# Kernel tuning notes

Measured on AMD Instinct MI355X. Metric: run time of the kernel, lower is better.

The kernel has to match this reference:

```python
import jax, jax.numpy as jnp
import numpy as np

B, T, H = 2048, 784, 64
STATE_DIM = 1
IN_DIM = 1 + STATE_DIM  # concat([t, y])
INNER_LR = 0.01
NUM_GRAD_STEPS = 4


def _unif(k, shape, fan_in):
    lim = 1.0 / np.sqrt(fan_in)
    return jax.random.uniform(k, shape, jnp.float32, -lim, lim)


def setup_inputs() -> dict:
    key = jax.random.key(0)
    ks = jax.random.split(key, 8)
    ts = (jnp.arange(T, dtype=jnp.float32) / T)
    xs = jax.random.normal(ks[0], (B, T), jnp.float32)
    mask = jax.random.bernoulli(ks[1], 0.5, (B, T - 1))  # teacher-forcing draws
    # equinox Linear default init: U(-1/sqrt(fan_in), 1/sqrt(fan_in)) for W and b
    W1 = _unif(ks[2], (H, IN_DIM), IN_DIM)
    b1 = _unif(ks[3], (H,), IN_DIM)
    W2 = _unif(ks[4], (H, H), H)
    b2 = _unif(ks[5], (H,), H)
    W3 = _unif(ks[6], (STATE_DIM, H), H)
    b3 = _unif(ks[7], (STATE_DIM,), H)
    return {"ts": ts, "xs": xs, "mask": mask,
            "W1": W1, "b1": b1, "W2": W2, "b2": b2, "W3": W3, "b3": b3}


def _mlp(theta, t, y):
    # theta: tuple of (W1,b1,W2,b2,W3,b3); t, y scalars -> output (state_dim,)
    W1, b1, W2, b2, W3, b3 = theta
    h = jnp.stack([t, y])                # (2,)
    h = jnp.tanh(W1 @ h + b1)            # (H,)
    h = jnp.tanh(W2 @ h + b2)            # (H,)
    return W3 @ h + b3                   # (state_dim,)


def reference(ts, xs, mask, W1, b1, W2, b2, W3, b3):
    theta0 = (W1, b1, W2, b2, W3, b3)

    def forward(xs_row, mask_row):
        def step(carry, inp):
            theta, t_prev, x_hat, x_prev = carry
            x_true, t_curr, m = inp
            x_t = jnp.where(m, x_true, x_hat)  # bernoulli(0.5) teacher forcing

            def inner_loss(th):
                pred = _mlp(th, t_curr, x_prev)
                return jnp.mean((pred - x_t) ** 2)

            for _ in range(NUM_GRAD_STEPS):
                g = jax.grad(inner_loss)(theta)
                theta = jax.tree_util.tree_map(
                    lambda p, gr: p - INNER_LR * gr, theta, g)

            deltat = t_curr - t_prev
            x_hat_new = _mlp(theta, t_curr + deltat, x_true).squeeze()
            return (theta, t_curr, x_hat_new, x_true), x_hat_new

        init = (theta0, ts[0], xs_row[0], xs_row[0])
        _, x_hats = jax.lax.scan(step, init, (xs_row[1:], ts[1:], mask_row))
        return jnp.concatenate([xs_row[:1], x_hats], axis=0)  # (T,)

    return jax.vmap(forward)(xs, mask)  # (B, T)
```

## Files before the change

kernel.cpp:

```cpp
#include <hip/hip_runtime.h>
#include <math.h>


#define TT  784
#define HH  64
#define LR  0.01f

typedef _Float16 h2v __attribute__((ext_vector_type(2)));
#define FDOT2(a, b, c) __builtin_amdgcn_fdot2((a), (b), (c), false)
#define BC(f) __builtin_bit_cast(h2v, (f))

__device__ __forceinline__ float fast_tanh(float x) {
    float e = __builtin_amdgcn_exp2f(x * 2.885390081777926814f);
    float r = __builtin_amdgcn_rcpf(e + 1.0f);
    return fmaf(-2.0f, r, 1.0f);
}

template <int CTRL, int RMASK, bool BC_>
__device__ __forceinline__ float dpp_add(float x) {
    int t = __builtin_amdgcn_update_dpp(0, __builtin_bit_cast(int, x),
                                        CTRL, RMASK, 0xf, BC_);
    return x + __builtin_bit_cast(float, t);
}

__device__ __forceinline__ float wave_sum(float x) {
    x = dpp_add<0x111, 0xf, true>(x);
    x = dpp_add<0x112, 0xf, true>(x);
    x = dpp_add<0x114, 0xf, true>(x);
    x = dpp_add<0x118, 0xf, true>(x);
    x = dpp_add<0x142, 0xa, false>(x);
    x = dpp_add<0x143, 0xc, false>(x);
    return __builtin_bit_cast(float,
        __builtin_amdgcn_readlane(__builtin_bit_cast(int, x), 63));
}

__global__ __launch_bounds__(64, 2)
void ttt_kernel(const float* __restrict__ ts,
                const float* __restrict__ xs,
                const int*   __restrict__ mask,
                const float* __restrict__ W1,
                const float* __restrict__ b1,
                const float* __restrict__ W2,
                const float* __restrict__ b2,
                const float* __restrict__ W3,
                const float* __restrict__ b3,
                float* __restrict__ out)
{
    __shared__ __align__(16) _Float16 s_h1h[HH];
    __shared__ __align__(16) _Float16 s_dzh[HH];
    __shared__ float s_ts[TT];
    __shared__ float s_xs[TT];
    __shared__ int   s_mask[TT - 1];

    const int row  = blockIdx.x;
    const int lane = threadIdx.x;

    for (int i = lane; i < TT; i += HH) {
        s_ts[i] = ts[i];
        s_xs[i] = xs[row * TT + i];
    }
    for (int i = lane; i < TT - 1; i += HH) s_mask[i] = mask[row * (TT - 1) + i];

    float w1a = W1[2 * lane + 0];
    float w1b = W1[2 * lane + 1];
    float b1v = b1[lane];
    float b2v = b2[lane];
    float w3v = W3[lane];
    float b3v = b3[0];

    h2v w2r[HH / 2];
    h2v w2c[HH / 2];
#pragma unroll
    for (int k = 0; k < HH / 2; ++k) {
        w2r[k] = h2v{(_Float16)W2[lane * HH + 2 * k], (_Float16)W2[lane * HH + 2 * k + 1]};
        w2c[k] = h2v{(_Float16)W2[(2 * k) * HH + lane], (_Float16)W2[(2 * k + 1) * HH + lane]};
    }
    __syncthreads();

    const float4* h1v4 = (const float4*)s_h1h;
    const float4* dzv4 = (const float4*)s_dzh;

    float t_prev = s_ts[0];
    const float x0 = s_xs[0];
    float x_hat  = x0;
    float x_prev = x0;
    if (lane == 0) out[row * TT] = x0;

    float4 hr[8];
    float  h1f, h2f, predf;
    float  z1f;
    float  sdz1 = 0.f;
    float  tc = 0.f, x_true = 0.f, tin = 0.f, nls = 0.f;

    auto FWD_TAIL = [&]() {
        float a0 = 0.f, a1 = 0.f, a2 = 0.f, a3 = 0.f;
#pragma unroll
        for (int k = 0; k < 8; ++k) {
            float4 q = h1v4[k];
            hr[k] = q;
            a0 = FDOT2(w2r[4 * k + 0], BC(q.x), a0);
            a1 = FDOT2(w2r[4 * k + 1], BC(q.y), a1);
            a2 = FDOT2(w2r[4 * k + 2], BC(q.z), a2);
            a3 = FDOT2(w2r[4 * k + 3], BC(q.w), a3);
        }
        float z2 = ((a0 + a1) + (a2 + a3)) + b2v;
        h2f = fast_tanh(z2);
        predf = wave_sum(w3v * h2f) + b3v;
    };

    auto MERGED = [&](float xt, bool final_) {
        const float dl   = 2.0f * (predf - xt);
        const float dz2s = dl * w3v * (1.0f - h2f * h2f);
        s_dzh[lane] = (_Float16)dz2s;
        w3v = fmaf(-LR * dl, h2f, w3v);
        b3v -= LR * dl;
        b2v -= LR * dz2s;
        const _Float16 sd = (_Float16)(-LR * dz2s);
        const h2v sdv = h2v{sd, sd};
        const _Float16 sh = (_Float16)(-LR * h1f);
        const h2v shv = h2v{sh, sh};
#pragma unroll
        for (int k = 0; k < 8; ++k) {
            float4 o = hr[k];
            w2r[4 * k + 0] += sdv * BC(o.x);
            w2r[4 * k + 1] += sdv * BC(o.y);
            w2r[4 * k + 2] += sdv * BC(o.z);
            w2r[4 * k + 3] += sdv * BC(o.w);
        }
        float d0 = 0.f, d1 = 0.f, d2 = 0.f, d3 = 0.f;
#pragma unroll
        for (int k = 0; k < 8; ++k) {
            float4 q = dzv4[k];
            d0 = FDOT2(w2c[4 * k + 0], BC(q.x), d0);
            d1 = FDOT2(w2c[4 * k + 1], BC(q.y), d1);
            d2 = FDOT2(w2c[4 * k + 2], BC(q.z), d2);
            d3 = FDOT2(w2c[4 * k + 3], BC(q.w), d3);
        }
        const float dh1 = (d0 + d1) + (d2 + d3);
        const float dz1 = dh1 * (1.0f - h1f * h1f);
        sdz1 += dz1;
        if (!final_) {
            z1f = fmaf(nls, dz1, z1f);
        } else {
            w1a = fmaf(-LR * tc,     sdz1, w1a);
            w1b = fmaf(-LR * x_prev, sdz1, w1b);
            b1v = fmaf(-LR,          sdz1, b1v);
            z1f = fmaf(w1a, tin, fmaf(w1b, x_true, b1v));
        }
        h1f = fast_tanh(z1f);
        s_h1h[lane] = (_Float16)h1f;
#pragma unroll
        for (int k = 0; k < 8; ++k) {
            float4 q = dzv4[k];
            w2c[4 * k + 0] += shv * BC(q.x);
            w2c[4 * k + 1] += shv * BC(q.y);
            w2c[4 * k + 2] += shv * BC(q.z);
            w2c[4 * k + 3] += shv * BC(q.w);
        }
        float a0 = 0.f, a1 = 0.f, a2 = 0.f, a3 = 0.f;
#pragma unroll
        for (int k = 0; k < 8; ++k) {
            float4 q = h1v4[k];
            hr[k] = q;
            a0 = FDOT2(w2r[4 * k + 0], BC(q.x), a0);
            a1 = FDOT2(w2r[4 * k + 1], BC(q.y), a1);
            a2 = FDOT2(w2r[4 * k + 2], BC(q.z), a2);
            a3 = FDOT2(w2r[4 * k + 3], BC(q.w), a3);
        }
        float z2 = ((a0 + a1) + (a2 + a3)) + b2v;
        h2f = fast_tanh(z2);
        predf = wave_sum(w3v * h2f) + b3v;
    };

    z1f = fmaf(w1a, s_ts[1], fmaf(w1b, x0, b1v));
    h1f = fast_tanh(z1f);
    s_h1h[lane] = (_Float16)h1f;
    FWD_TAIL();

    for (int t = 1; t < TT; ++t) {
        tc     = s_ts[t];
        x_true = s_xs[t];
        tin    = tc + (tc - t_prev);
        nls    = -LR * fmaf(tc, tc, fmaf(x_prev, x_prev, 1.0f));
        const float x_t = s_mask[t - 1] ? x_true : x_hat;

        sdz1 = 0.f;
        MERGED(x_t, false);
        MERGED(x_t, false);
        MERGED(x_t, false);
        MERGED(x_t, true);
        x_hat = predf;

        if (lane == 0) out[row * TT + t] = x_hat;
        t_prev = tc;
        x_prev = x_true;
    }
}

extern "C" void kernel_launch(void* const* d_in, const int* in_sizes, int n_in,
                              void* d_out, int out_size, void* d_ws, size_t ws_size,
                              hipStream_t stream) {
    const float* ts   = (const float*)d_in[0];
    const float* xs   = (const float*)d_in[1];
    const int*   mask = (const int*)d_in[2];
    const float* W1   = (const float*)d_in[3];
    const float* b1   = (const float*)d_in[4];
    const float* W2   = (const float*)d_in[5];
    const float* b2   = (const float*)d_in[6];
    const float* W3   = (const float*)d_in[7];
    const float* b3   = (const float*)d_in[8];
    float* out = (float*)d_out;

    const int B = in_sizes[1] / TT;
    dim3 grid(B), block(HH);
    hipLaunchKernelGGL(ttt_kernel, grid, block, 0, stream,
                       ts, xs, mask, W1, b1, W2, b2, W3, b3, out);
}
```

Measured before the change: 2.523 ms.

## Factor loss scalar out of backward vector, fuse W2 updates, buffer outputs in LDS

```diff
diff --git a/kernel.cpp b/kernel.cpp
--- a/kernel.cpp
+++ b/kernel.cpp
@@ -9,6 +9,7 @@
 typedef _Float16 h2v __attribute__((ext_vector_type(2)));
 #define FDOT2(a, b, c) __builtin_amdgcn_fdot2((a), (b), (c), false)
 #define BC(f) __builtin_bit_cast(h2v, (f))
+#define PKFMA(acc, a, b) acc = __builtin_elementwise_fma((a), (b), (acc))
 
 __device__ __forceinline__ float fast_tanh(float x) {
     float e = __builtin_amdgcn_exp2f(x * 2.885390081777926814f);
@@ -47,9 +48,10 @@
                 float* __restrict__ out)
 {
     __shared__ __align__(16) _Float16 s_h1h[HH];
-    __shared__ __align__(16) _Float16 s_dzh[HH];
+    __shared__ __align__(16) _Float16 s_uh[HH];
     __shared__ float s_ts[TT];
     __shared__ float s_xs[TT];
+    __shared__ float s_out[TT];
     __shared__ int   s_mask[TT - 1];
 
     const int row  = blockIdx.x;
@@ -78,66 +80,48 @@
     __syncthreads();
 
     const float4* h1v4 = (const float4*)s_h1h;
-    const float4* dzv4 = (const float4*)s_dzh;
+    const float4* uv4  = (const float4*)s_uh;
 
     float t_prev = s_ts[0];
     const float x0 = s_xs[0];
     float x_hat  = x0;
     float x_prev = x0;
-    if (lane == 0) out[row * TT] = x0;
+    if (lane == 0) s_out[0] = x0;
 
     float4 hr[8];
     float  h1f, h2f, predf;
+    float  ul;
     float  z1f;
     float  sdz1 = 0.f;
     float  tc = 0.f, x_true = 0.f, tin = 0.f, nls = 0.f;
 
-    auto FWD_TAIL = [&]() {
-        float a0 = 0.f, a1 = 0.f, a2 = 0.f, a3 = 0.f;
-#pragma unroll
-        for (int k = 0; k < 8; ++k) {
-            float4 q = h1v4[k];
-            hr[k] = q;
-            a0 = FDOT2(w2r[4 * k + 0], BC(q.x), a0);
-            a1 = FDOT2(w2r[4 * k + 1], BC(q.y), a1);
-            a2 = FDOT2(w2r[4 * k + 2], BC(q.z), a2);
-            a3 = FDOT2(w2r[4 * k + 3], BC(q.w), a3);
-        }
-        float z2 = ((a0 + a1) + (a2 + a3)) + b2v;
-        h2f = fast_tanh(z2);
-        predf = wave_sum(w3v * h2f) + b3v;
-    };
-
     auto MERGED = [&](float xt, bool final_) {
-        const float dl   = 2.0f * (predf - xt);
-        const float dz2s = dl * w3v * (1.0f - h2f * h2f);
-        s_dzh[lane] = (_Float16)dz2s;
-        w3v = fmaf(-LR * dl, h2f, w3v);
-        b3v -= LR * dl;
-        b2v -= LR * dz2s;
-        const _Float16 sd = (_Float16)(-LR * dz2s);
+        const float diff = predf - xt;
+        const float dl   = diff + diff;
+        const float ndl  = -LR * dl;
+        w3v = fmaf(ndl, h2f, w3v);
+        b3v += ndl;
+        b2v = fmaf(ndl, ul, b2v);
+        const _Float16 sd = (_Float16)(ndl * ul);
         const h2v sdv = h2v{sd, sd};
-        const _Float16 sh = (_Float16)(-LR * h1f);
+        const _Float16 sh = (_Float16)(ndl * h1f);
         const h2v shv = h2v{sh, sh};
-#pragma unroll
-        for (int k = 0; k < 8; ++k) {
-            float4 o = hr[k];
-            w2r[4 * k + 0] += sdv * BC(o.x);
-            w2r[4 * k + 1] += sdv * BC(o.y);
-            w2r[4 * k + 2] += sdv * BC(o.z);
-            w2r[4 * k + 3] += sdv * BC(o.w);
-        }
         float d0 = 0.f, d1 = 0.f, d2 = 0.f, d3 = 0.f;
 #pragma unroll
         for (int k = 0; k < 8; ++k) {
-            float4 q = dzv4[k];
+            float4 q = uv4[k];
             d0 = FDOT2(w2c[4 * k + 0], BC(q.x), d0);
             d1 = FDOT2(w2c[4 * k + 1], BC(q.y), d1);
             d2 = FDOT2(w2c[4 * k + 2], BC(q.z), d2);
             d3 = FDOT2(w2c[4 * k + 3], BC(q.w), d3);
-        }
-        const float dh1 = (d0 + d1) + (d2 + d3);
-        const float dz1 = dh1 * (1.0f - h1f * h1f);
+            PKFMA(w2c[4 * k + 0], shv, BC(q.x));
+            PKFMA(w2c[4 * k + 1], shv, BC(q.y));
+            PKFMA(w2c[4 * k + 2], shv, BC(q.z));
+            PKFMA(w2c[4 * k + 3], shv, BC(q.w));
+        }
+        const float raw = (d0 + d1) + (d2 + d3);
+        const float dh1 = dl * raw;
+        const float dz1 = dh1 * fmaf(-h1f, h1f, 1.0f);
         sdz1 += dz1;
         if (!final_) {
             z1f = fmaf(nls, dz1, z1f);
@@ -151,13 +135,13 @@
         s_h1h[lane] = (_Float16)h1f;
 #pragma unroll
         for (int k = 0; k < 8; ++k) {
-            float4 q = dzv4[k];
-            w2c[4 * k + 0] += shv * BC(q.x);
-            w2c[4 * k + 1] += shv * BC(q.y);
-            w2c[4 * k + 2] += shv * BC(q.z);
-            w2c[4 * k + 3] += shv * BC(q.w);
-        }
-        float a0 = 0.f, a1 = 0.f, a2 = 0.f, a3 = 0.f;
+            float4 o = hr[k];
+            PKFMA(w2r[4 * k + 0], sdv, BC(o.x));
+            PKFMA(w2r[4 * k + 1], sdv, BC(o.y));
+            PKFMA(w2r[4 * k + 2], sdv, BC(o.z));
+            PKFMA(w2r[4 * k + 3], sdv, BC(o.w));
+        }
+        float a0 = b2v, a1 = 0.f, a2 = 0.f, a3 = 0.f;
 #pragma unroll
         for (int k = 0; k < 8; ++k) {
             float4 q = h1v4[k];
@@ -167,15 +151,35 @@
             a2 = FDOT2(w2r[4 * k + 2], BC(q.z), a2);
             a3 = FDOT2(w2r[4 * k + 3], BC(q.w), a3);
         }
-        float z2 = ((a0 + a1) + (a2 + a3)) + b2v;
+        const float z2 = (a0 + a1) + (a2 + a3);
         h2f = fast_tanh(z2);
+        const float uf = w3v * fmaf(-h2f, h2f, 1.0f);
+        ul = uf;
+        s_uh[lane] = (_Float16)uf;
         predf = wave_sum(w3v * h2f) + b3v;
     };
 
     z1f = fmaf(w1a, s_ts[1], fmaf(w1b, x0, b1v));
     h1f = fast_tanh(z1f);
     s_h1h[lane] = (_Float16)h1f;
-    FWD_TAIL();
+    {
+        float a0 = b2v, a1 = 0.f, a2 = 0.f, a3 = 0.f;
+#pragma unroll
+        for (int k = 0; k < 8; ++k) {
+            float4 q = h1v4[k];
+            hr[k] = q;
+            a0 = FDOT2(w2r[4 * k + 0], BC(q.x), a0);
+            a1 = FDOT2(w2r[4 * k + 1], BC(q.y), a1);
+            a2 = FDOT2(w2r[4 * k + 2], BC(q.z), a2);
+            a3 = FDOT2(w2r[4 * k + 3], BC(q.w), a3);
+        }
+        const float z2 = (a0 + a1) + (a2 + a3);
+        h2f = fast_tanh(z2);
+        const float uf = w3v * fmaf(-h2f, h2f, 1.0f);
+        ul = uf;
+        s_uh[lane] = (_Float16)uf;
+        predf = wave_sum(w3v * h2f) + b3v;
+    }
 
     for (int t = 1; t < TT; ++t) {
         tc     = s_ts[t];
@@ -191,10 +195,12 @@
         MERGED(x_t, true);
         x_hat = predf;
 
-        if (lane == 0) out[row * TT + t] = x_hat;
+        if (lane == 0) s_out[t] = x_hat;
         t_prev = tc;
         x_prev = x_true;
     }
+
+    for (int i = lane; i < TT; i += HH) out[row * TT + i] = s_out[i];
 }
 
 extern "C" void kernel_launch(void* const* d_in, const int* in_sizes, int n_in,
```

Result: no change. 2.518 ms (-0.2%).

## Process two batch rows per wavefront with interleaved dependent chains

Applied to the files above, without the earlier changes.

```diff
diff --git a/kernel.cpp b/kernel.cpp
--- a/kernel.cpp
+++ b/kernel.cpp
@@ -9,6 +9,7 @@
 typedef _Float16 h2v __attribute__((ext_vector_type(2)));
 #define FDOT2(a, b, c) __builtin_amdgcn_fdot2((a), (b), (c), false)
 #define BC(f) __builtin_bit_cast(h2v, (f))
+#define PKFMA(acc, a, b) acc = __builtin_elementwise_fma((a), (b), (acc))
 
 __device__ __forceinline__ float fast_tanh(float x) {
     float e = __builtin_amdgcn_exp2f(x * 2.885390081777926814f);
@@ -34,7 +35,7 @@
         __builtin_amdgcn_readlane(__builtin_bit_cast(int, x), 63));
 }
 
-__global__ __launch_bounds__(64, 2)
+__global__ __launch_bounds__(64, 1)
 void ttt_kernel(const float* __restrict__ ts,
                 const float* __restrict__ xs,
                 const int*   __restrict__ mask,
@@ -46,154 +47,234 @@
                 const float* __restrict__ b3,
                 float* __restrict__ out)
 {
-    __shared__ __align__(16) _Float16 s_h1h[HH];
-    __shared__ __align__(16) _Float16 s_dzh[HH];
+    __shared__ __align__(16) _Float16 s_h1h[2][HH];
+    __shared__ __align__(16) _Float16 s_uh[2][HH];
     __shared__ float s_ts[TT];
-    __shared__ float s_xs[TT];
-    __shared__ int   s_mask[TT - 1];
-
-    const int row  = blockIdx.x;
+    __shared__ float s_xs[2][TT];
+    __shared__ float s_out[2][TT];
+    __shared__ int   s_mask[2][TT - 1];
+
+    const int rowA = 2 * blockIdx.x;
+    const int rowB = rowA + 1;
     const int lane = threadIdx.x;
 
     for (int i = lane; i < TT; i += HH) {
-        s_ts[i] = ts[i];
-        s_xs[i] = xs[row * TT + i];
-    }
-    for (int i = lane; i < TT - 1; i += HH) s_mask[i] = mask[row * (TT - 1) + i];
-
-    float w1a = W1[2 * lane + 0];
-    float w1b = W1[2 * lane + 1];
-    float b1v = b1[lane];
-    float b2v = b2[lane];
-    float w3v = W3[lane];
-    float b3v = b3[0];
-
-    h2v w2r[HH / 2];
-    h2v w2c[HH / 2];
+        s_ts[i]    = ts[i];
+        s_xs[0][i] = xs[rowA * TT + i];
+        s_xs[1][i] = xs[rowB * TT + i];
+    }
+    for (int i = lane; i < TT - 1; i += HH) {
+        s_mask[0][i] = mask[rowA * (TT - 1) + i];
+        s_mask[1][i] = mask[rowB * (TT - 1) + i];
+    }
+
+    float w1aA = W1[2 * lane + 0], w1aB = w1aA;
+    float w1bA = W1[2 * lane + 1], w1bB = w1bA;
+    float b1vA = b1[lane], b1vB = b1vA;
+    float b2vA = b2[lane], b2vB = b2vA;
+    float w3vA = W3[lane], w3vB = w3vA;
+    float b3vA = b3[0],    b3vB = b3vA;
+
+    h2v w2rA[HH / 2], w2rB[HH / 2];
+    h2v w2cA[HH / 2], w2cB[HH / 2];
 #pragma unroll
     for (int k = 0; k < HH / 2; ++k) {
-        w2r[k] = h2v{(_Float16)W2[lane * HH + 2 * k], (_Float16)W2[lane * HH + 2 * k + 1]};
-        w2c[k] = h2v{(_Float16)W2[(2 * k) * HH + lane], (_Float16)W2[(2 * k + 1) * HH + lane]};
+        h2v r = h2v{(_Float16)W2[lane * HH + 2 * k], (_Float16)W2[lane * HH + 2 * k + 1]};
+        h2v c = h2v{(_Float16)W2[(2 * k) * HH + lane], (_Float16)W2[(2 * k + 1) * HH + lane]};
+        w2rA[k] = r; w2rB[k] = r;
+        w2cA[k] = c; w2cB[k] = c;
     }
     __syncthreads();
 
-    const float4* h1v4 = (const float4*)s_h1h;
-    const float4* dzv4 = (const float4*)s_dzh;
+    const float4* h1v4A = (const float4*)s_h1h[0];
+    const float4* h1v4B = (const float4*)s_h1h[1];
+    const float4* uv4A  = (const float4*)s_uh[0];
+    const float4* uv4B  = (const float4*)s_uh[1];
 
     float t_prev = s_ts[0];
-    const float x0 = s_xs[0];
-    float x_hat  = x0;
-    float x_prev = x0;
-    if (lane == 0) out[row * TT] = x0;
-
-    float4 hr[8];
-    float  h1f, h2f, predf;
-    float  z1f;
-    float  sdz1 = 0.f;
-    float  tc = 0.f, x_true = 0.f, tin = 0.f, nls = 0.f;
-
-    auto FWD_TAIL = [&]() {
-        float a0 = 0.f, a1 = 0.f, a2 = 0.f, a3 = 0.f;
-#pragma unroll
-        for (int k = 0; k < 8; ++k) {
-            float4 q = h1v4[k];
-            hr[k] = q;
-            a0 = FDOT2(w2r[4 * k + 0], BC(q.x), a0);
-            a1 = FDOT2(w2r[4 * k + 1], BC(q.y), a1);
-            a2 = FDOT2(w2r[4 * k + 2], BC(q.z), a2);
-            a3 = FDOT2(w2r[4 * k + 3], BC(q.w), a3);
-        }
-        float z2 = ((a0 + a1) + (a2 + a3)) + b2v;
-        h2f = fast_tanh(z2);
-        predf = wave_sum(w3v * h2f) + b3v;
+    const float x0A = s_xs[0][0];
+    const float x0B = s_xs[1][0];
+    float x_hatA = x0A, x_prevA = x0A;
+    float x_hatB = x0B, x_prevB = x0B;
+    if (lane == 0) { s_out[0][0] = x0A; s_out[1][0] = x0B; }
+
+    float4 hrA[8], hrB[8];
+    float  h1fA, h2fA, predA, ulA, z1fA, sdz1A = 0.f;
+    float  h1fB, h2fB, predB, ulB, z1fB, sdz1B = 0.f;
+    float  tc = 0.f, tin = 0.f;
+    float  x_trueA = 0.f, nlsA = 0.f;
+    float  x_trueB = 0.f, nlsB = 0.f;
+
+    auto MERGED2 = [&](float xtA, float xtB, bool final_) {
+        const float diffA = predA - xtA;
+        const float dlA   = diffA + diffA;
+        const float ndlA  = -LR * dlA;
+        const float diffB = predB - xtB;
+        const float dlB   = diffB + diffB;
+        const float ndlB  = -LR * dlB;
+        w3vA = fmaf(ndlA, h2fA, w3vA);  b3vA += ndlA;  b2vA = fmaf(ndlA, ulA, b2vA);
+        w3vB = fmaf(ndlB, h2fB, w3vB);  b3vB += ndlB;  b2vB = fmaf(ndlB, ulB, b2vB);
+        const _Float16 sdA = (_Float16)(ndlA * ulA);   const h2v sdvA = h2v{sdA, sdA};
+        const _Float16 shA = (_Float16)(ndlA * h1fA);  const h2v shvA = h2v{shA, shA};
+        const _Float16 sdB = (_Float16)(ndlB * ulB);   const h2v sdvB = h2v{sdB, sdB};
+        const _Float16 shB = (_Float16)(ndlB * h1fB);  const h2v shvB = h2v{shB, shB};
+        float dA0 = 0.f, dA1 = 0.f, dA2 = 0.f, dA3 = 0.f;
+        float dB0 = 0.f, dB1 = 0.f, dB2 = 0.f, dB3 = 0.f;
+#pragma unroll
+        for (int k = 0; k < 8; ++k) {
+            float4 qa = uv4A[k];
+            float4 qb = uv4B[k];
+            dA0 = FDOT2(w2cA[4 * k + 0], BC(qa.x), dA0);
+            dA1 = FDOT2(w2cA[4 * k + 1], BC(qa.y), dA1);
+            dA2 = FDOT2(w2cA[4 * k + 2], BC(qa.z), dA2);
+            dA3 = FDOT2(w2cA[4 * k + 3], BC(qa.w), dA3);
+            dB0 = FDOT2(w2cB[4 * k + 0], BC(qb.x), dB0);
+            dB1 = FDOT2(w2cB[4 * k + 1], BC(qb.y), dB1);
+            dB2 = FDOT2(w2cB[4 * k + 2], BC(qb.z), dB2);
+            dB3 = FDOT2(w2cB[4 * k + 3], BC(qb.w), dB3);
+            PKFMA(w2cA[4 * k + 0], shvA, BC(qa.x));
+            PKFMA(w2cA[4 * k + 1], shvA, BC(qa.y));
+            PKFMA(w2cA[4 * k + 2], shvA, BC(qa.z));
+            PKFMA(w2cA[4 * k + 3], shvA, BC(qa.w));
+            PKFMA(w2cB[4 * k + 0], shvB, BC(qb.x));
+            PKFMA(w2cB[4 * k + 1], shvB, BC(qb.y));
+            PKFMA(w2cB[4 * k + 2], shvB, BC(qb.z));
+            PKFMA(w2cB[4 * k + 3], shvB, BC(qb.w));
+        }
+        const float rawA = (dA0 + dA1) + (dA2 + dA3);
+        const float dh1A = dlA * rawA;
+        const float dz1A = dh1A * fmaf(-h1fA, h1fA, 1.0f);
+        sdz1A += dz1A;
+        const float rawB = (dB0 + dB1) + (dB2 + dB3);
+        const float dh1B = dlB * rawB;
+        const float dz1B = dh1B * fmaf(-h1fB, h1fB, 1.0f);
+        sdz1B += dz1B;
+        if (!final_) {
+            z1fA = fmaf(nlsA, dz1A, z1fA);
+            z1fB = fmaf(nlsB, dz1B, z1fB);
+        } else {
+            w1aA = fmaf(-LR * tc,      sdz1A, w1aA);
+            w1bA = fmaf(-LR * x_prevA, sdz1A, w1bA);
+            b1vA = fmaf(-LR,           sdz1A, b1vA);
+            z1fA = fmaf(w1aA, tin, fmaf(w1bA, x_trueA, b1vA));
+            w1aB = fmaf(-LR * tc,      sdz1B, w1aB);
+            w1bB = fmaf(-LR * x_prevB, sdz1B, w1bB);
+            b1vB = fmaf(-LR,           sdz1B, b1vB);
+            z1fB = fmaf(w1aB, tin, fmaf(w1bB, x_trueB, b1vB));
+        }
+        h1fA = fast_tanh(z1fA);
+        s_h1h[0][lane] = (_Float16)h1fA;
+        h1fB = fast_tanh(z1fB);
+        s_h1h[1][lane] = (_Float16)h1fB;
+#pragma unroll
+        for (int k = 0; k < 8; ++k) {
+            float4 oa = hrA[k];
+            float4 ob = hrB[k];
+            PKFMA(w2rA[4 * k + 0], sdvA, BC(oa.x));
+            PKFMA(w2rA[4 * k + 1], sdvA, BC(oa.y));
+            PKFMA(w2rA[4 * k + 2], sdvA, BC(oa.z));
+            PKFMA(w2rA[4 * k + 3], sdvA, BC(oa.w));
+            PKFMA(w2rB[4 * k + 0], sdvB, BC(ob.x));
+            PKFMA(w2rB[4 * k + 1], sdvB, BC(ob.y));
+            PKFMA(w2rB[4 * k + 2], sdvB, BC(ob.z));
+            PKFMA(w2rB[4 * k + 3], sdvB, BC(ob.w));
+        }
+        float aA0 = b2vA, aA1 = 0.f, aA2 = 0.f, aA3 = 0.f;
+        float aB0 = b2vB, aB1 = 0.f, aB2 = 0.f, aB3 = 0.f;
+#pragma unroll
+        for (int k = 0; k < 8; ++k) {
+            float4 qa = h1v4A[k];
+            float4 qb = h1v4B[k];
+            hrA[k] = qa;
+            hrB[k] = qb;
+            aA0 = FDOT2(w2rA[4 * k + 0], BC(qa.x), aA0);
+            aA1 = FDOT2(w2rA[4 * k + 1], BC(qa.y), aA1);
+            aA2 = FDOT2(w2rA[4 * k + 2], BC(qa.z), aA2);
+            aA3 = FDOT2(w2rA[4 * k + 3], BC(qa.w), aA3);
+            aB0 = FDOT2(w2rB[4 * k + 0], BC(qb.x), aB0);
+            aB1 = FDOT2(w2rB[4 * k + 1], BC(qb.y), aB1);
+            aB2 = FDOT2(w2rB[4 * k + 2], BC(qb.z), aB2);
+            aB3 = FDOT2(w2rB[4 * k + 3], BC(qb.w), aB3);
+        }
+        const float z2A = (aA0 + aA1) + (aA2 + aA3);
+        h2fA = fast_tanh(z2A);
+        const float ufA = w3vA * fmaf(-h2fA, h2fA, 1.0f);
+        ulA = ufA;
+        s_uh[0][lane] = (_Float16)ufA;
+        const float z2B = (aB0 + aB1) + (aB2 + aB3);
+        h2fB = fast_tanh(z2B);
+        const float ufB = w3vB * fmaf(-h2fB, h2fB, 1.0f);
+        ulB = ufB;
+        s_uh[1][lane] = (_Float16)ufB;
+        predA = wave_sum(w3vA * h2fA) + b3vA;
+        predB = wave_sum(w3vB * h2fB) + b3vB;
     };
 
-    auto MERGED = [&](float xt, bool final_) {
-        const float dl   = 2.0f * (predf - xt);
-        const float dz2s = dl * w3v * (1.0f - h2f * h2f);
-        s_dzh[lane] = (_Float16)dz2s;
-        w3v = fmaf(-LR * dl, h2f, w3v);
-        b3v -= LR * dl;
-        b2v -= LR * dz2s;
-        const _Float16 sd = (_Float16)(-LR * dz2s);
-        const h2v sdv = h2v{sd, sd};
-        const _Float16 sh = (_Float16)(-LR * h1f);
-        const h2v shv = h2v{sh, sh};
-#pragma unroll
-        for (int k = 0; k < 8; ++k) {
-            float4 o = hr[k];
-            w2r[4 * k + 0] += sdv * BC(o.x);
-            w2r[4 * k + 1] += sdv * BC(o.y);
-            w2r[4 * k + 2] += sdv * BC(o.z);
-            w2r[4 * k + 3] += sdv * BC(o.w);
-        }
-        float d0 = 0.f, d1 = 0.f, d2 = 0.f, d3 = 0.f;
-#pragma unroll
-        for (int k = 0; k < 8; ++k) {
-            float4 q = dzv4[k];
-            d0 = FDOT2(w2c[4 * k + 0], BC(q.x), d0);
-            d1 = FDOT2(w2c[4 * k + 1], BC(q.y), d1);
-            d2 = FDOT2(w2c[4 * k + 2], BC(q.z), d2);
-            d3 = FDOT2(w2c[4 * k + 3], BC(q.w), d3);
-        }
-        const float dh1 = (d0 + d1) + (d2 + d3);
-        const float dz1 = dh1 * (1.0f - h1f * h1f);
-        sdz1 += dz1;
-        if (!final_) {
-            z1f = fmaf(nls, dz1, z1f);
-        } else {
-            w1a = fmaf(-LR * tc,     sdz1, w1a);
-            w1b = fmaf(-LR * x_prev, sdz1, w1b);
-            b1v = fmaf(-LR,          sdz1, b1v);
-            z1f = fmaf(w1a, tin, fmaf(w1b, x_true, b1v));
-        }
-        h1f = fast_tanh(z1f);
-        s_h1h[lane] = (_Float16)h1f;
-#pragma unroll
-        for (int k = 0; k < 8; ++k) {
-            float4 q = dzv4[k];
-            w2c[4 * k + 0] += shv * BC(q.x);
-            w2c[4 * k + 1] += shv * BC(q.y);
-            w2c[4 * k + 2] += shv * BC(q.z);
-            w2c[4 * k + 3] += shv * BC(q.w);
-        }
-        float a0 = 0.f, a1 = 0.f, a2 = 0.f, a3 = 0.f;
-#pragma unroll
-        for (int k = 0; k < 8; ++k) {
-            float4 q = h1v4[k];
-            hr[k] = q;
-            a0 = FDOT2(w2r[4 * k + 0], BC(q.x), a0);
-            a1 = FDOT2(w2r[4 * k + 1], BC(q.y), a1);
-            a2 = FDOT2(w2r[4 * k + 2], BC(q.z), a2);
-            a3 = FDOT2(w2r[4 * k + 3], BC(q.w), a3);
-        }
-        float z2 = ((a0 + a1) + (a2 + a3)) + b2v;
-        h2f = fast_tanh(z2);
-        predf = wave_sum(w3v * h2f) + b3v;
-    };
-
-    z1f = fmaf(w1a, s_ts[1], fmaf(w1b, x0, b1v));
-    h1f = fast_tanh(z1f);
-    s_h1h[lane] = (_Float16)h1f;
-    FWD_TAIL();
+    z1fA = fmaf(w1aA, s_ts[1], fmaf(w1bA, x0A, b1vA));
+    h1fA = fast_tanh(z1fA);
+    s_h1h[0][lane] = (_Float16)h1fA;
+    z1fB = fmaf(w1aB, s_ts[1], fmaf(w1bB, x0B, b1vB));
+    h1fB = fast_tanh(z1fB);
+    s_h1h[1][lane] = (_Float16)h1fB;
+    {
+        float aA0 = b2vA, aA1 = 0.f, aA2 = 0.f, aA3 = 0.f;
+        float aB0 = b2vB, aB1 = 0.f, aB2 = 0.f, aB3 = 0.f;
+#pragma unroll
+        for (int k = 0; k < 8; ++k) {
+            float4 qa = h1v4A[k];
+            float4 qb = h1v4B[k];
+            hrA[k] = qa;
+            hrB[k] = qb;
+            aA0 = FDOT2(w2rA[4 * k + 0], BC(qa.x), aA0);
+            aA1 = FDOT2(w2rA[4 * k + 1], BC(qa.y), aA1);
+            aA2 = FDOT2(w2rA[4 * k + 2], BC(qa.z), aA2);
+            aA3 = FDOT2(w2rA[4 * k + 3], BC(qa.w), aA3);
+            aB0 = FDOT2(w2rB[4 * k + 0], BC(qb.x), aB0);
+            aB1 = FDOT2(w2rB[4 * k + 1], BC(qb.y), aB1);
+            aB2 = FDOT2(w2rB[4 * k + 2], BC(qb.z), aB2);
+            aB3 = FDOT2(w2rB[4 * k + 3], BC(qb.w), aB3);
+        }
+        const float z2A = (aA0 + aA1) + (aA2 + aA3);
+        h2fA = fast_tanh(z2A);
+        const float ufA = w3vA * fmaf(-h2fA, h2fA, 1.0f);
+        ulA = ufA;
+        s_uh[0][lane] = (_Float16)ufA;
+        const float z2B = (aB0 + aB1) + (aB2 + aB3);
+        h2fB = fast_tanh(z2B);
+        const float ufB = w3vB * fmaf(-h2fB, h2fB, 1.0f);
+        ulB = ufB;
+        s_uh[1][lane] = (_Float16)ufB;
+        predA = wave_sum(w3vA * h2fA) + b3vA;
+        predB = wave_sum(w3vB * h2fB) + b3vB;
+    }
 
     for (int t = 1; t < TT; ++t) {
-        tc     = s_ts[t];
-        x_true = s_xs[t];
-        tin    = tc + (tc - t_prev);
-        nls    = -LR * fmaf(tc, tc, fmaf(x_prev, x_prev, 1.0f));
-        const float x_t = s_mask[t - 1] ? x_true : x_hat;
-
-        sdz1 = 0.f;
-        MERGED(x_t, false);
-        MERGED(x_t, false);
-        MERGED(x_t, false);
-        MERGED(x_t, true);
-        x_hat = predf;
-
-        if (lane == 0) out[row * TT + t] = x_hat;
-        t_prev = tc;
-        x_prev = x_true;
+        tc      = s_ts[t];
+        tin     = tc + (tc - t_prev);
+        x_trueA = s_xs[0][t];
+        x_trueB = s_xs[1][t];
+        nlsA = -LR * fmaf(tc, tc, fmaf(x_prevA, x_prevA, 1.0f));
+        nlsB = -LR * fmaf(tc, tc, fmaf(x_prevB, x_prevB, 1.0f));
+        const float x_tA = s_mask[0][t - 1] ? x_trueA : x_hatA;
+        const float x_tB = s_mask[1][t - 1] ? x_trueB : x_hatB;
+
+        sdz1A = 0.f;  sdz1B = 0.f;
+        MERGED2(x_tA, x_tB, false);
+        MERGED2(x_tA, x_tB, false);
+        MERGED2(x_tA, x_tB, false);
+        MERGED2(x_tA, x_tB, true);
+        x_hatA = predA;
+        x_hatB = predB;
+
+        if (lane == 0) { s_out[0][t] = x_hatA; s_out[1][t] = x_hatB; }
+        t_prev  = tc;
+        x_prevA = x_trueA;
+        x_prevB = x_trueB;
+    }
+
+    for (int i = lane; i < TT; i += HH) {
+        out[rowA * TT + i] = s_out[0][i];
+        out[rowB * TT + i] = s_out[1][i];
     }
 }
 
@@ -212,7 +293,7 @@
     float* out = (float*)d_out;
 
     const int B = in_sizes[1] / TT;
-    dim3 grid(B), block(HH);
+    dim3 grid(B / 2), block(HH);
     hipLaunchKernelGGL(ttt_kernel, grid, block, 0, stream,
                        ts, xs, mask, W1, b1, W2, b2, W3, b3, out);
 }
```

Measured after the change: 3.386 ms. +34.2%, slower.
